# Optimization experiments

Measured on AMD Instinct MI355X. Metric: run time of the kernel, lower is better.

Reference implementation:

```python
import jax, jax.numpy as jnp
import numpy as np

N_NODES = 100000
N_EDGES = 1000000
D_IN = 64
D_OUT = 64


def setup_inputs() -> dict:
    key = jax.random.key(0)
    k1, k2, k3, k4 = jax.random.split(key, 4)
    x = jax.random.normal(k1, (N_NODES, D_IN), dtype=jnp.float32)
    edge_index = jax.random.randint(k2, (2, N_EDGES), 0, N_NODES, dtype=jnp.int64)
    edge_weight = jax.random.uniform(k3, (N_EDGES,), dtype=jnp.float32)
    W = jax.random.normal(k4, (D_OUT, D_IN), dtype=jnp.float32) * (1.0 / np.sqrt(D_IN))
    bias = jnp.zeros((D_OUT,), dtype=jnp.float32)
    return {"x": x, "edge_index": edge_index, "edge_weight": edge_weight, "W": W, "bias": bias}


def reference(x, edge_index, edge_weight, W, bias):
    n = x.shape[0]
    self_loops = jnp.arange(n)
    row = jnp.concatenate([edge_index[0], self_loops])  # [E+N]
    col = jnp.concatenate([edge_index[1], self_loops])  # [E+N]
    ew = jnp.concatenate([edge_weight, jnp.ones((n,), x.dtype)])  # [E+N]
    # degree via scatter-add of edge weights into row nodes
    deg = jax.ops.segment_sum(ew, row, num_segments=n)  # [N]
    deg_safe = jnp.where(deg > 0, deg, 1.0)
    deg_inv_sqrt = jnp.where(deg > 0, jax.lax.rsqrt(deg_safe), 0.0)  # inf -> 0
    norm = deg_inv_sqrt[row] * ew * deg_inv_sqrt[col]  # [E+N]
    # gather-scale-scatter aggregation
    msg = x[col] * norm[:, None]  # [E+N, D_IN]
    out = jax.ops.segment_sum(msg, row, num_segments=n)  # [N, D_IN]
    return out @ W.T + bias
```

## Files before the change

kernel.cpp:

```cpp
#include <hip/hip_runtime.h>
#include <hip/hip_bf16.h>

#define D 64
#define M44 ((1ULL << 44) - 1)
#define SPILLCAP 65536

typedef __attribute__((ext_vector_type(4))) _Float16 half4;
typedef __attribute__((ext_vector_type(8))) _Float16 half8;

template <int KS>
__global__ __launch_bounds__(256) void k_build(const int* __restrict__ rowi,
                                               const int* __restrict__ coli,
                                               const float* __restrict__ ew,
                                               unsigned long long* __restrict__ packed,
                                               unsigned int* __restrict__ slots,
                                               int4* __restrict__ spill,
                                               int* __restrict__ spillCnt, int nE,
                                               int prepBlocks,
                                               const float4* __restrict__ x4,
                                               half8* __restrict__ xh8, int nv) {
    int b = blockIdx.x;
    if (b < prepBlocks) {
        int t = b * 256 + threadIdx.x;
        if (t >= nv) return;
        float4 a = x4[2 * t], bb = x4[2 * t + 1];
        half8 h;
        h[0] = (_Float16)a.x; h[1] = (_Float16)a.y; h[2] = (_Float16)a.z; h[3] = (_Float16)a.w;
        h[4] = (_Float16)bb.x; h[5] = (_Float16)bb.y; h[6] = (_Float16)bb.z; h[7] = (_Float16)bb.w;
        xh8[t] = h;
        return;
    }
    int bp = b - prepBlocks;
    int p = bp & 7;
    int e = (bp >> 3) * 256 + threadIdx.x;
    if (e >= nE) return;
    int r = rowi[e];
    if ((r & 7) != p) return;
    int c = coli[e];
    float w = ew[e];
    unsigned long long fx = (unsigned long long)((double)w * 4294967296.0);
    unsigned long long old = atomicAdd(&packed[r], (1ULL << 44) | fx);
    int rank = (int)(old >> 44);
    if (rank < KS) {
        int q = (int)(w * 32768.0f + 0.5f);
        if (q > 32767) q = 32767;
        slots[r * KS + rank] = ((unsigned int)c << 15) | (unsigned int)q;
    } else {
        int pI = atomicAdd(spillCnt, 1);
        if (pI < SPILLCAP) spill[pI] = make_int4(r, c, __float_as_int(w), 0);
    }
}

__device__ __forceinline__ float dis_of(unsigned long long pk) {
    return rsqrtf(1.0f + (float)(pk & M44) * (1.0f / 4294967296.0f));
}

__global__ __launch_bounds__(256) void k_scale(const unsigned long long* __restrict__ packed,
                                               half8* __restrict__ xh8, int nv8) {
    int t = blockIdx.x * 256 + threadIdx.x;
    if (t >= nv8) return;
    float dis = dis_of(packed[t >> 3]);
    half8 h = xh8[t];
#pragma unroll
    for (int k = 0; k < 8; ++k) h[k] = (_Float16)((float)h[k] * dis);
    xh8[t] = h;
}

template <int KS, bool H>
__global__ __launch_bounds__(256) void k_gather_gemm(const float* __restrict__ x,
                                                     const _Float16* __restrict__ xh,
                                                     const unsigned long long* __restrict__ packed,
                                                     const unsigned int* __restrict__ slots,
                                                     const int4* __restrict__ spill,
                                                     const int* __restrict__ spillCnt,
                                                     const float* __restrict__ W,
                                                     const float* __restrict__ bias,
                                                     float* __restrict__ out, int n) {
    __shared__ float Bs[D * D];
    __shared__ float Ast[16 * D];
    float4* Ast4 = (float4*)Ast;
    int tid = threadIdx.x;

    const float4* W4 = (const float4*)W;
#pragma unroll
    for (int v = 0; v < 4; ++v) {
        int idx = tid + v * 256;
        int o  = idx >> 4;
        int kc = idx & 15;
        float4 wv = W4[idx];
        int gq = o >> 2, oo = o & 3;
        int cpos = 4 * ((gq + kc) & 15) + oo;
        Bs[(4 * kc + 0) * 64 + cpos] = wv.x;
        Bs[(4 * kc + 1) * 64 + cpos] = wv.y;
        Bs[(4 * kc + 2) * 64 + cpos] = wv.z;
        Bs[(4 * kc + 3) * 64 + cpos] = wv.w;
    }

    int j   = tid & 15;
    int grp = tid >> 4;
    int cls = blockIdx.x & 7;
    int q   = blockIdx.x >> 3;
    int i   = ((q * 16 + grp) << 3) + cls;

    float4 acc = make_float4(0.f, 0.f, 0.f, 0.f);
    const float4* x4 = (const float4*)x;
    const half4*  xh4 = (const half4*)xh;
    if (i < n) {
        unsigned long long pk = packed[i];
        half4 hi; float4 xi;
        if constexpr (H) hi = xh4[i * 16 + j]; else xi = x4[i * 16 + j];
        int rawc = (int)(pk >> 44);
        int c_n = rawc < KS ? rawc : KS;
        int s = i * KS;
        for (int off = 0; off < c_n; off += 16) {
            int idx = off + j;
            unsigned int rec = 0u;
            float wj = 0.f;
            if (idx < c_n) {
                rec = slots[s + idx];
                if constexpr (!H)
                    wj = (float)(rec & 32767u) * (1.0f / 32768.0f) * dis_of(packed[rec >> 15]);
            }
#pragma unroll
            for (int t = 0; t < 16; ++t) {
                unsigned int rt = (unsigned int)__shfl((int)rec, t, 16);
                int col = (int)(rt >> 15);
                if constexpr (H) {
                    float w = (float)(rt & 32767u) * (1.0f / 32768.0f);
                    half4 hv = xh4[col * 16 + j];
                    acc.x += w * (float)hv[0]; acc.y += w * (float)hv[1];
                    acc.z += w * (float)hv[2]; acc.w += w * (float)hv[3];
                } else {
                    float w = __shfl(wj, t, 16);
                    float4 xv = x4[col * 16 + j];
                    acc.x += w * xv.x; acc.y += w * xv.y;
                    acc.z += w * xv.z; acc.w += w * xv.w;
                }
            }
        }
        if (rawc > KS) {
            int total = *spillCnt;
            if (total > SPILLCAP) total = SPILLCAP;
            for (int sp = 0; sp < total; ++sp) {
                int4 v = spill[sp];
                if (v.x == i) {
                    if constexpr (H) {
                        float w = __int_as_float(v.z);
                        half4 hv = xh4[v.y * 16 + j];
                        acc.x += w * (float)hv[0]; acc.y += w * (float)hv[1];
                        acc.z += w * (float)hv[2]; acc.w += w * (float)hv[3];
                    } else {
                        float w = __int_as_float(v.z) * dis_of(packed[v.y]);
                        float4 xv = x4[v.y * 16 + j];
                        acc.x += w * xv.x; acc.y += w * xv.y;
                        acc.z += w * xv.z; acc.w += w * xv.w;
                    }
                }
            }
        }
        float di = dis_of(pk);
        if constexpr (H) {
            acc.x = di * ((float)hi[0] + acc.x);
            acc.y = di * ((float)hi[1] + acc.y);
            acc.z = di * ((float)hi[2] + acc.z);
            acc.w = di * ((float)hi[3] + acc.w);
        } else {
            acc.x = di * (di * xi.x + acc.x);
            acc.y = di * (di * xi.y + acc.y);
            acc.z = di * (di * xi.z + acc.z);
            acc.w = di * (di * xi.w + acc.w);
        }
    }
    Ast4[grp * 16 + ((j + (grp >> 2)) & 15)] = acc;
    __syncthreads();

    int row = tid >> 4;
    int cg  = tid & 15;
    float4 oacc = ((const float4*)bias)[cg];
#pragma unroll 4
    for (int kc = 0; kc < 16; ++kc) {
        float4 a4 = Ast4[row * 16 + ((kc + (row >> 2)) & 15)];
        int cp = 4 * ((cg + kc) & 15);
        float4 b0 = *(const float4*)&Bs[(4 * kc + 0) * 64 + cp];
        float4 b1 = *(const float4*)&Bs[(4 * kc + 1) * 64 + cp];
        float4 b2 = *(const float4*)&Bs[(4 * kc + 2) * 64 + cp];
        float4 b3 = *(const float4*)&Bs[(4 * kc + 3) * 64 + cp];
        oacc.x += a4.x * b0.x + a4.y * b1.x + a4.z * b2.x + a4.w * b3.x;
        oacc.y += a4.x * b0.y + a4.y * b1.y + a4.z * b2.y + a4.w * b3.y;
        oacc.z += a4.x * b0.z + a4.y * b1.z + a4.z * b2.z + a4.w * b3.z;
        oacc.w += a4.x * b0.w + a4.y * b1.w + a4.z * b2.w + a4.w * b3.w;
    }
    int r = ((q * 16 + row) << 3) + cls;
    if (r < n) ((float4*)out)[r * 16 + cg] = oacc;
}

extern "C" void kernel_launch(void* const* d_in, const int* in_sizes, int n_in,
                              void* d_out, int out_size, void* d_ws, size_t ws_size,
                              hipStream_t stream) {
    const float* x    = (const float*)d_in[0];
    const int*   ei   = (const int*)d_in[1];
    const float* ew   = (const float*)d_in[2];
    const float* W    = (const float*)d_in[3];
    const float* bias = (const float*)d_in[4];
    float* out = (float*)d_out;

    int n  = in_sizes[0] / D;
    int nE = in_sizes[2];
    const int* rowi = ei;
    const int* coli = ei + nE;

    char* base = (char*)d_ws;
    size_t off_packed = 0;
    size_t off_spillCnt = ((size_t)n * 8 + 127) & ~(size_t)127;
    size_t off_slots = off_spillCnt + 128;
    auto mkNeed = [&](int KS, int withH) {
        size_t o = off_slots + (size_t)n * KS * 4 + (size_t)SPILLCAP * 16;
        return o + (withH ? (size_t)n * D * 2 : 0);
    };

    int KS, useH;
    if (ws_size >= mkNeed(32, 1))      { KS = 32; useH = 1; }
    else if (ws_size >= mkNeed(24, 1)) { KS = 24; useH = 1; }
    else                               { KS = 24; useH = 0; }

    unsigned long long* packed = (unsigned long long*)(base + off_packed);
    int* spillCnt = (int*)(base + off_spillCnt);
    unsigned int* slots = (unsigned int*)(base + off_slots);
    int4* spill = (int4*)(base + off_slots + (size_t)n * KS * 4);
    _Float16* xh = (_Float16*)(base + off_slots + (size_t)n * KS * 4 + (size_t)SPILLCAP * 16);

    int gE = (nE + 255) / 256;
    int buildBlocks = gE * 8;
    int nv = n * D / 8;
    int prepBlocks = useH ? ((((nv + 255) / 256) + 7) & ~7) : 0;
    int nPerClass = (n + 7) / 8;
    int gT = 8 * ((nPerClass + 15) / 16);
    int nv8 = n * 8;

    hipMemsetAsync(packed, 0, off_slots, stream);
    if (KS == 32) {
        k_build<32><<<prepBlocks + buildBlocks, 256, 0, stream>>>(
            rowi, coli, ew, packed, slots, spill, spillCnt, nE,
            prepBlocks, (const float4*)x, (half8*)xh, nv);
        k_scale<<<(nv8 + 255) / 256, 256, 0, stream>>>(packed, (half8*)xh, nv8);
        k_gather_gemm<32, true><<<gT, 256, 0, stream>>>(x, xh, packed, slots, spill, spillCnt, W, bias, out, n);
    } else if (useH) {
        k_build<24><<<prepBlocks + buildBlocks, 256, 0, stream>>>(
            rowi, coli, ew, packed, slots, spill, spillCnt, nE,
            prepBlocks, (const float4*)x, (half8*)xh, nv);
        k_scale<<<(nv8 + 255) / 256, 256, 0, stream>>>(packed, (half8*)xh, nv8);
        k_gather_gemm<24, true><<<gT, 256, 0, stream>>>(x, xh, packed, slots, spill, spillCnt, W, bias, out, n);
    } else {
        k_build<24><<<buildBlocks, 256, 0, stream>>>(
            rowi, coli, ew, packed, slots, spill, spillCnt, nE,
            0, (const float4*)x, (half8*)xh, nv);
        k_gather_gemm<24, false><<<gT, 256, 0, stream>>>(x, xh, packed, slots, spill, spillCnt, W, bias, out, n);
    }
}
```

Measured before the change: 177.6 us.

## Process two nodes per 16-lane group in gather-GEMM kernel

Each 256-thread block of the fused gather+GEMM kernel now handles 32 nodes instead of 16. Every 16-lane group gathers neighbours for two nodes with independent accumulators, and the grid is halved. The point is to keep more independent memory loads in flight per thread and to spread the per-block cost of staging W into shared memory over twice as many output rows. In exchange, register use and shared memory for the staging tile go up, the block count drops, and the per-node loops are serialised inside each group.

Result: slower. 187.6 us (+5.6%).

```diff
diff --git a/kernel.cpp b/kernel.cpp
--- a/kernel.cpp
+++ b/kernel.cpp
@@ -66,6 +66,29 @@
     xh8[t] = h;
 }
 
+template <bool H>
+__device__ __forceinline__ void batch16(unsigned int rec, float wj, int j,
+                                        const half4* __restrict__ xh4,
+                                        const float4* __restrict__ x4,
+                                        float4& acc) {
+#pragma unroll
+    for (int t = 0; t < 16; ++t) {
+        unsigned int rt = (unsigned int)__shfl((int)rec, t, 16);
+        int col = (int)(rt >> 15);
+        if constexpr (H) {
+            float w = (float)(rt & 32767u) * (1.0f / 32768.0f);
+            half4 hv = xh4[col * 16 + j];
+            acc.x += w * (float)hv[0]; acc.y += w * (float)hv[1];
+            acc.z += w * (float)hv[2]; acc.w += w * (float)hv[3];
+        } else {
+            float w = __shfl(wj, t, 16);
+            float4 xv = x4[col * 16 + j];
+            acc.x += w * xv.x; acc.y += w * xv.y;
+            acc.z += w * xv.z; acc.w += w * xv.w;
+        }
+    }
+}
+
 template <int KS, bool H>
 __global__ __launch_bounds__(256) void k_gather_gemm(const float* __restrict__ x,
                                                      const _Float16* __restrict__ xh,
@@ -77,7 +100,7 @@
                                                      const float* __restrict__ bias,
                                                      float* __restrict__ out, int n) {
     __shared__ float Bs[D * D];
-    __shared__ float Ast[16 * D];
+    __shared__ float Ast[32 * D];
     float4* Ast4 = (float4*)Ast;
     int tid = threadIdx.x;
 
@@ -100,98 +123,123 @@
     int grp = tid >> 4;
     int cls = blockIdx.x & 7;
     int q   = blockIdx.x >> 3;
-    int i   = ((q * 16 + grp) << 3) + cls;
-
-    float4 acc = make_float4(0.f, 0.f, 0.f, 0.f);
+    int liA = q * 32 + grp;
+    int iA  = (liA << 3) + cls;
+    int iB  = ((liA + 16) << 3) + cls;
+    bool vA = iA < n, vB = iB < n;
+
     const float4* x4 = (const float4*)x;
     const half4*  xh4 = (const half4*)xh;
-    if (i < n) {
-        unsigned long long pk = packed[i];
-        half4 hi; float4 xi;
-        if constexpr (H) hi = xh4[i * 16 + j]; else xi = x4[i * 16 + j];
-        int rawc = (int)(pk >> 44);
-        int c_n = rawc < KS ? rawc : KS;
-        int s = i * KS;
-        for (int off = 0; off < c_n; off += 16) {
-            int idx = off + j;
-            unsigned int rec = 0u;
-            float wj = 0.f;
-            if (idx < c_n) {
-                rec = slots[s + idx];
-                if constexpr (!H)
-                    wj = (float)(rec & 32767u) * (1.0f / 32768.0f) * dis_of(packed[rec >> 15]);
-            }
-#pragma unroll
-            for (int t = 0; t < 16; ++t) {
-                unsigned int rt = (unsigned int)__shfl((int)rec, t, 16);
-                int col = (int)(rt >> 15);
+    float4 accA = make_float4(0.f, 0.f, 0.f, 0.f);
+    float4 accB = make_float4(0.f, 0.f, 0.f, 0.f);
+
+    unsigned long long pkA = vA ? packed[iA] : 0ULL;
+    unsigned long long pkB = vB ? packed[iB] : 0ULL;
+    half4 hiA{}, hiB{}; float4 xiA = accA, xiB = accA;
+    if (vA) { if constexpr (H) hiA = xh4[iA * 16 + j]; else xiA = x4[iA * 16 + j]; }
+    if (vB) { if constexpr (H) hiB = xh4[iB * 16 + j]; else xiB = x4[iB * 16 + j]; }
+    int rawA = (int)(pkA >> 44), rawB = (int)(pkB >> 44);
+    int cA = rawA < KS ? rawA : KS;
+    int cB = rawB < KS ? rawB : KS;
+    unsigned int recA = 0u, recB = 0u;
+    float wjA = 0.f, wjB = 0.f;
+    if (j < cA) {
+        recA = slots[iA * KS + j];
+        if constexpr (!H) wjA = (float)(recA & 32767u) * (1.0f / 32768.0f) * dis_of(packed[recA >> 15]);
+    }
+    if (j < cB) {
+        recB = slots[iB * KS + j];
+        if constexpr (!H) wjB = (float)(recB & 32767u) * (1.0f / 32768.0f) * dis_of(packed[recB >> 15]);
+    }
+    batch16<H>(recA, wjA, j, xh4, x4, accA);
+    batch16<H>(recB, wjB, j, xh4, x4, accB);
+    for (int off = 16; off < cA; off += 16) {
+        unsigned int r2 = 0u; float w2 = 0.f;
+        if (off + j < cA) {
+            r2 = slots[iA * KS + off + j];
+            if constexpr (!H) w2 = (float)(r2 & 32767u) * (1.0f / 32768.0f) * dis_of(packed[r2 >> 15]);
+        }
+        batch16<H>(r2, w2, j, xh4, x4, accA);
+    }
+    for (int off = 16; off < cB; off += 16) {
+        unsigned int r2 = 0u; float w2 = 0.f;
+        if (off + j < cB) {
+            r2 = slots[iB * KS + off + j];
+            if constexpr (!H) w2 = (float)(r2 & 32767u) * (1.0f / 32768.0f) * dis_of(packed[r2 >> 15]);
+        }
+        batch16<H>(r2, w2, j, xh4, x4, accB);
+    }
+    if (rawA > KS || rawB > KS) {
+        int total = *spillCnt;
+        if (total > SPILLCAP) total = SPILLCAP;
+        for (int sp = 0; sp < total; ++sp) {
+            int4 v = spill[sp];
+            float4* acc = (v.x == iA) ? &accA : (v.x == iB ? &accB : nullptr);
+            if (acc) {
                 if constexpr (H) {
-                    float w = (float)(rt & 32767u) * (1.0f / 32768.0f);
-                    half4 hv = xh4[col * 16 + j];
-                    acc.x += w * (float)hv[0]; acc.y += w * (float)hv[1];
-                    acc.z += w * (float)hv[2]; acc.w += w * (float)hv[3];
+                    float w = __int_as_float(v.z);
+                    half4 hv = xh4[v.y * 16 + j];
+                    acc->x += w * (float)hv[0]; acc->y += w * (float)hv[1];
+                    acc->z += w * (float)hv[2]; acc->w += w * (float)hv[3];
                 } else {
-                    float w = __shfl(wj, t, 16);
-                    float4 xv = x4[col * 16 + j];
-                    acc.x += w * xv.x; acc.y += w * xv.y;
-                    acc.z += w * xv.z; acc.w += w * xv.w;
+                    float w = __int_as_float(v.z) * dis_of(packed[v.y]);
+                    float4 xv = x4[v.y * 16 + j];
+                    acc->x += w * xv.x; acc->y += w * xv.y;
+                    acc->z += w * xv.z; acc->w += w * xv.w;
                 }
             }
         }
-        if (rawc > KS) {
-            int total = *spillCnt;
-            if (total > SPILLCAP) total = SPILLCAP;
-            for (int sp = 0; sp < total; ++sp) {
-                int4 v = spill[sp];
-                if (v.x == i) {
-                    if constexpr (H) {
-                        float w = __int_as_float(v.z);
-                        half4 hv = xh4[v.y * 16 + j];
-                        acc.x += w * (float)hv[0]; acc.y += w * (float)hv[1];
-                        acc.z += w * (float)hv[2]; acc.w += w * (float)hv[3];
-                    } else {
-                        float w = __int_as_float(v.z) * dis_of(packed[v.y]);
-                        float4 xv = x4[v.y * 16 + j];
-                        acc.x += w * xv.x; acc.y += w * xv.y;
-                        acc.z += w * xv.z; acc.w += w * xv.w;
-                    }
-                }
-            }
-        }
-        float di = dis_of(pk);
+    }
+    if (vA) {
+        float di = dis_of(pkA);
         if constexpr (H) {
-            acc.x = di * ((float)hi[0] + acc.x);
-            acc.y = di * ((float)hi[1] + acc.y);
-            acc.z = di * ((float)hi[2] + acc.z);
-            acc.w = di * ((float)hi[3] + acc.w);
+            accA.x = di * ((float)hiA[0] + accA.x); accA.y = di * ((float)hiA[1] + accA.y);
+            accA.z = di * ((float)hiA[2] + accA.z); accA.w = di * ((float)hiA[3] + accA.w);
         } else {
-            acc.x = di * (di * xi.x + acc.x);
-            acc.y = di * (di * xi.y + acc.y);
-            acc.z = di * (di * xi.z + acc.z);
-            acc.w = di * (di * xi.w + acc.w);
-        }
-    }
-    Ast4[grp * 16 + ((j + (grp >> 2)) & 15)] = acc;
+            accA.x = di * (di * xiA.x + accA.x); accA.y = di * (di * xiA.y + accA.y);
+            accA.z = di * (di * xiA.z + accA.z); accA.w = di * (di * xiA.w + accA.w);
+        }
+    }
+    if (vB) {
+        float di = dis_of(pkB);
+        if constexpr (H) {
+            accB.x = di * ((float)hiB[0] + accB.x); accB.y = di * ((float)hiB[1] + accB.y);
+            accB.z = di * ((float)hiB[2] + accB.z); accB.w = di * ((float)hiB[3] + accB.w);
+        } else {
+            accB.x = di * (di * xiB.x + accB.x); accB.y = di * (di * xiB.y + accB.y);
+            accB.z = di * (di * xiB.z + accB.z); accB.w = di * (di * xiB.w + accB.w);
+        }
+    }
+    Ast4[grp * 16 + ((j + (grp >> 2)) & 15)] = accA;
+    Ast4[(grp + 16) * 16 + ((j + ((grp + 16) >> 2)) & 15)] = accB;
     __syncthreads();
 
     int row = tid >> 4;
     int cg  = tid & 15;
-    float4 oacc = ((const float4*)bias)[cg];
+    float4 o1 = ((const float4*)bias)[cg];
+    float4 o2 = o1;
 #pragma unroll 4
     for (int kc = 0; kc < 16; ++kc) {
-        float4 a4 = Ast4[row * 16 + ((kc + (row >> 2)) & 15)];
+        float4 a1 = Ast4[row * 16 + ((kc + (row >> 2)) & 15)];
+        float4 a2 = Ast4[(row + 16) * 16 + ((kc + ((row + 16) >> 2)) & 15)];
         int cp = 4 * ((cg + kc) & 15);
         float4 b0 = *(const float4*)&Bs[(4 * kc + 0) * 64 + cp];
         float4 b1 = *(const float4*)&Bs[(4 * kc + 1) * 64 + cp];
         float4 b2 = *(const float4*)&Bs[(4 * kc + 2) * 64 + cp];
         float4 b3 = *(const float4*)&Bs[(4 * kc + 3) * 64 + cp];
-        oacc.x += a4.x * b0.x + a4.y * b1.x + a4.z * b2.x + a4.w * b3.x;
-        oacc.y += a4.x * b0.y + a4.y * b1.y + a4.z * b2.y + a4.w * b3.y;
-        oacc.z += a4.x * b0.z + a4.y * b1.z + a4.z * b2.z + a4.w * b3.z;
-        oacc.w += a4.x * b0.w + a4.y * b1.w + a4.z * b2.w + a4.w * b3.w;
-    }
-    int r = ((q * 16 + row) << 3) + cls;
-    if (r < n) ((float4*)out)[r * 16 + cg] = oacc;
+        o1.x += a1.x * b0.x + a1.y * b1.x + a1.z * b2.x + a1.w * b3.x;
+        o1.y += a1.x * b0.y + a1.y * b1.y + a1.z * b2.y + a1.w * b3.y;
+        o1.z += a1.x * b0.z + a1.y * b1.z + a1.z * b2.z + a1.w * b3.z;
+        o1.w += a1.x * b0.w + a1.y * b1.w + a1.z * b2.w + a1.w * b3.w;
+        o2.x += a2.x * b0.x + a2.y * b1.x + a2.z * b2.x + a2.w * b3.x;
+        o2.y += a2.x * b0.y + a2.y * b1.y + a2.z * b2.y + a2.w * b3.y;
+        o2.z += a2.x * b0.z + a2.y * b1.z + a2.z * b2.z + a2.w * b3.z;
+        o2.w += a2.x * b0.w + a2.y * b1.w + a2.z * b2.w + a2.w * b3.w;
+    }
+    int r1 = ((q * 32 + row) << 3) + cls;
+    int r2 = ((q * 32 + 16 + row) << 3) + cls;
+    if (r1 < n) ((float4*)out)[r1 * 16 + cg] = o1;
+    if (r2 < n) ((float4*)out)[r2 * 16 + cg] = o2;
 }
 
 extern "C" void kernel_launch(void* const* d_in, const int* in_sizes, int n_in,
@@ -210,7 +258,6 @@
     const int* coli = ei + nE;
 
     char* base = (char*)d_ws;
-    size_t off_packed = 0;
     size_t off_spillCnt = ((size_t)n * 8 + 127) & ~(size_t)127;
     size_t off_slots = off_spillCnt + 128;
     auto mkNeed = [&](int KS, int withH) {
@@ -223,7 +270,7 @@
     else if (ws_size >= mkNeed(24, 1)) { KS = 24; useH = 1; }
     else                               { KS = 24; useH = 0; }
 
-    unsigned long long* packed = (unsigned long long*)(base + off_packed);
+    unsigned long long* packed = (unsigned long long*)base;
     int* spillCnt = (int*)(base + off_spillCnt);
     unsigned int* slots = (unsigned int*)(base + off_slots);
     int4* spill = (int4*)(base + off_slots + (size_t)n * KS * 4);
@@ -234,7 +281,7 @@
     int nv = n * D / 8;
     int prepBlocks = useH ? ((((nv + 255) / 256) + 7) & ~7) : 0;
     int nPerClass = (n + 7) / 8;
-    int gT = 8 * ((nPerClass + 15) / 16);
+    int gT = 8 * ((nPerClass + 31) / 32);
     int nv8 = n * 8;
 
     hipMemsetAsync(packed, 0, off_slots, stream);
```
